# Kernel tuning notes

Hardware: AMD Instinct MI355X
Metric: run time of the kernel (lower is better)

The kernel has to match this reference:

```python
import jax, jax.numpy as jnp
import numpy as np
import math

SR = 16000
WIN = 320
HOP = 160
NFFT = 512
NMEL = 64
PREEMPH = 0.97
LOG_GUARD = 2.0 ** (-24)
PAD_TO = 16
EPS = 1e-5  # CONSTANT added to std


def _slaney_mel_fbanks(sr=SR, n_fft=NFFT, n_mels=NMEL, fmin=0.0, fmax=8000.0):
    """Replicates torchaudio.functional.melscale_fbanks(norm='slaney', mel_scale='slaney').
    Returns [n_mels, n_freqs] (already transposed like the torch buffer `fb`)."""
    n_freqs = n_fft // 2 + 1
    all_freqs = np.linspace(0.0, sr / 2.0, n_freqs)
    f_sp = 200.0 / 3.0
    min_log_hz = 1000.0
    min_log_mel = min_log_hz / f_sp
    logstep = math.log(6.4) / 27.0

    def hz2mel(f):
        f = np.asarray(f, dtype=np.float64)
        return np.where(f >= min_log_hz,
                        min_log_mel + np.log(np.maximum(f, 1e-10) / min_log_hz) / logstep,
                        f / f_sp)

    def mel2hz(m):
        m = np.asarray(m, dtype=np.float64)
        return np.where(m >= min_log_mel,
                        min_log_hz * np.exp(logstep * (m - min_log_mel)),
                        f_sp * m)

    m_pts = np.linspace(hz2mel(fmin), hz2mel(fmax), n_mels + 2)
    f_pts = mel2hz(m_pts)                       # [n_mels+2]
    f_diff = f_pts[1:] - f_pts[:-1]             # [n_mels+1]
    slopes = f_pts[None, :] - all_freqs[:, None]  # [n_freqs, n_mels+2]
    down = -slopes[:, :-2] / f_diff[:-1]
    up = slopes[:, 2:] / f_diff[1:]
    fb = np.maximum(0.0, np.minimum(down, up))  # [n_freqs, n_mels]
    enorm = 2.0 / (f_pts[2:] - f_pts[:-2])      # slaney area normalization
    fb = fb * enorm[None, :]
    return fb.T.astype(np.float32)              # [n_mels, n_freqs]


def _hann_window_padded(win_length=WIN, n_fft=NFFT):
    # the window symmetrically to n_fft.
    w = np.hanning(win_length).astype(np.float32)
    left = (n_fft - win_length) // 2
    out = np.zeros(n_fft, dtype=np.float32)
    out[left:left + win_length] = w
    return out


def setup_inputs() -> dict:
    key = jax.random.key(0)
    kx, kl = jax.random.split(key)
    B, L = 32, 256000
    x = jax.random.normal(kx, (B, L), dtype=jnp.float32)
    # ragged valid lengths in [L/2, L] (plenty of frames per feature)
    seq_len = jax.random.randint(kl, (B,), L // 2, L + 1, dtype=jnp.int32)
    window = jnp.asarray(_hann_window_padded())       # [NFFT]
    fb = jnp.asarray(_slaney_mel_fbanks())            # [NMEL, NFFT//2+1]
    return {"x": x, "seq_len": seq_len, "window": window, "fb": fb}


def _forward(x, seq_len, window, fb):
    B, L = x.shape
    # get_seq_len: pad_amount = 2*(n_fft//2); floor((L + pad - n_fft)/hop) + 1
    feat_len = (seq_len + NFFT - NFFT) // HOP + 1     # = seq_len // HOP + 1
    # pre-emphasis
    x = jnp.concatenate([x[:, :1], x[:, 1:] - PREEMPH * x[:, :-1]], axis=1)
    # STFT, center=True reflect padding (eval mode: no dither)
    pad = NFFT // 2
    xp = jnp.pad(x, ((0, 0), (pad, pad)), mode='reflect')
    T = L // HOP + 1                                  # 1601 frames
    idx = jnp.arange(T)[:, None] * HOP + jnp.arange(NFFT)[None, :]
    frames = xp[:, idx] * window                      # [B, T, NFFT]
    spec = jnp.fft.rfft(frames, axis=-1)              # [B, T, F]
    # magnitude then mag_power=2 -> power spectrum (guard=0 since use_grads=False)
    pow_spec = spec.real ** 2 + spec.imag ** 2        # [B, T, F]
    mel = jnp.einsum('mf,btf->bmt', fb, pow_spec)     # [B, NMEL, T]
    logmel = jnp.log(mel + LOG_GUARD)
    # per_feature masked normalization (torch.std is unbiased -> /(n-1)), std += 1e-5
    mask = (jnp.arange(T)[None, :] < feat_len[:, None])          # [B, T]
    m = mask[:, None, :].astype(logmel.dtype)                    # [B, 1, T]
    n = feat_len.astype(logmel.dtype)[:, None, None]
    mean = jnp.sum(logmel * m, axis=2, keepdims=True) / n
    var = jnp.sum(((logmel - mean) * m) ** 2, axis=2, keepdims=True) / (n - 1.0)
    std = jnp.sqrt(var) + EPS
    out = (logmel - mean) / std
    # fill padding frames with pad_value=0
    out = jnp.where(m > 0, out, 0.0)
    # pad time dim to a multiple of pad_to=16 with pad_value
    pad_amt = (-T) % PAD_TO
    out = jnp.pad(out, ((0, 0), (0, 0), (0, pad_amt)), constant_values=0.0)
    return out, feat_len


def reference(x, seq_len, window, fb):
    return _forward(x, seq_len, window, fb)
```

## Files before the change

kernel.cpp:

```cpp
#include <hip/hip_runtime.h>
#include <math.h>

#define L_IN 256000
#define T_FR 1601
#define T_PAD 1616
#define NMEL_K 64
#define F_BINS 257
#define HOP_K 160
#define PRE_E 0.97f
#define LOG_GUARD_K 5.9604644775390625e-08f
#define FPB 16
#define CONC 4
#define GROUPS 101
#define SPAN 2912

__device__ __forceinline__ float2 cmulf(float2 a, float2 b) {
  return make_float2(a.x * b.x - a.y * b.y, a.x * b.y + a.y * b.x);
}

__device__ __forceinline__ float dpp_xor1(float x) {
  return __int_as_float(__builtin_amdgcn_mov_dpp(__float_as_int(x), 0xB1, 0xF, 0xF, true));
}
__device__ __forceinline__ float dpp_xor2(float x) {
  return __int_as_float(__builtin_amdgcn_mov_dpp(__float_as_int(x), 0x4E, 0xF, 0xF, true));
}

__global__ void prep_kernel(const float* __restrict__ fb, float* __restrict__ fbc,
                            int* __restrict__ loAl, float* __restrict__ rsum,
                            float* __restrict__ rsumsq) {
  const int m = blockIdx.x;
  const int t = threadIdx.x;
  if (t < 32) {
    rsum[m * 32 + t] = 0.0f;
    rsumsq[m * 32 + t] = 0.0f;
  }
  int first = 512, last = -1;
  for (int c = 0; c < 5; ++c) {
    int f = t + 64 * c;
    if (f < F_BINS) {
      float v = fb[m * F_BINS + f];
      if (v > 0.0f) { first = min(first, f); last = max(last, f); }
    }
  }
  for (int off = 32; off > 0; off >>= 1) {
    first = min(first, __shfl_xor(first, off));
    last = max(last, __shfl_xor(last, off));
  }
  int lo = (first <= last) ? first : 0;
  int lastv = (first <= last) ? last : 0;
  int la = lo & ~3;
  if (t == 0) loAl[m] = la;
  if (t < 32) {
    int f = la + t;
    float v = (f >= lo && f <= lastv && f < F_BINS) ? fb[m * F_BINS + f] : 0.0f;
    fbc[m * 32 + t] = v;
  }
}

#define FFT_STAGE(I, PR, PI)                                        \
  {                                                                 \
    const int H__ = 32 >> (I);                                      \
    const bool hi__ = (lane & H__) != 0;                            \
    const float cc__ = stc[I], ss__ = sts[I];                       \
    _Pragma("unroll")                                               \
    for (int r = 0; r < 4; ++r) {                                   \
      float tr = (PR), ti = (PI);                                   \
      float sr = Br[r] + tr, si = Bi[r] + ti;                       \
      float dr = tr - Br[r], di = ti - Bi[r];                       \
      float pr = dr * cc__ - di * ss__, pi = dr * ss__ + di * cc__; \
      Br[r] = hi__ ? pr : sr;                                       \
      Bi[r] = hi__ ? pi : si;                                       \
    }                                                               \
  }

__global__ void __launch_bounds__(256) frame_fft_mel_kernel(
    const float* __restrict__ x, const int* __restrict__ seq_len,
    const float* __restrict__ window, const float* __restrict__ fbc,
    const int* __restrict__ loAl, float* __restrict__ out,
    float* __restrict__ rsum, float* __restrict__ rsumsq) {
  __shared__ __align__(16) float xs[SPAN];
  __shared__ __align__(16) float pw[CONC][288];
  __shared__ float outm[NMEL_K][FPB + 1];

  const int tid = threadIdx.x;
  const int w = tid >> 6;
  const int lane = tid & 63;
  const int b = blockIdx.x / GROUPS;
  const int g = blockIdx.x - b * GROUPS;
  const int t0 = g * FPB;
  const float* xb = x + (size_t)b * L_IN;
  const int base = t0 * HOP_K - 256;
  const int fl = seq_len[b] / HOP_K + 1;

  if (base >= 0 && base + SPAN <= L_IN) {
    const float4* xb4 = (const float4*)(xb + base);
    float4* xs4 = (float4*)xs;
    for (int s4 = tid; s4 < SPAN / 4; s4 += 256) {
      float4 cur = xb4[s4];
      float prev = xb[base + 4 * s4 - 1];
      float4 o;
      o.x = fmaf(-PRE_E, prev, cur.x);
      o.y = fmaf(-PRE_E, cur.x, cur.y);
      o.z = fmaf(-PRE_E, cur.y, cur.z);
      o.w = fmaf(-PRE_E, cur.z, cur.w);
      xs4[s4] = o;
    }
  } else {
    for (int n = tid; n < SPAN; n += 256) {
      int i = base + n;
      i = (i < 0) ? -i : i;
      i = (i >= L_IN) ? (2 * L_IN - 2 - i) : i;
      xs[n] = (i == 0) ? xb[0] : fmaf(-PRE_E, xb[i - 1], xb[i]);
    }
  }

  if (lane >= 33 && lane < 64) pw[w][224 + lane] = 0.0f;

  const int sig = __builtin_bitreverse32(lane) >> 26;
  float wr[4], wi[4];
#pragma unroll
  for (int q = 0; q < 4; ++q) {
    float2 wv = *(const float2*)(window + 2 * (lane + 64 * q));
    wr[q] = wv.x; wi[q] = wv.y;
  }
  float2 tw1, tw2, tw3;
  {
    float a = -0.024543692606170259f * (float)lane;
    __sincosf(a, &tw1.y, &tw1.x);
    tw2 = cmulf(tw1, tw1);
    tw3 = cmulf(tw2, tw1);
  }
  float stc[6], sts[6];
#pragma unroll
  for (int i = 0; i < 6; ++i) {
    int H = 32 >> i;
    int p = lane & (H - 1);
    float a = -3.14159265358979323846f * (float)p / (float)H;
    __sincosf(a, &sts[i], &stc[i]);
  }
  float cu[4], su[4];
  {
    float a = -0.049087385212340519f * (float)sig;
    float cb, sb;
    __sincosf(a, &sb, &cb);
    const float C[4] = {1.0f, 0.99992470183914454f, 0.99969881869620425f, 0.99932238458834954f};
    const float S[4] = {0.0f, 0.01227153828571993f, 0.02454122852291229f, 0.03680722294135883f};
#pragma unroll
    for (int r = 0; r < 4; ++r) {
      cu[r] = cb * C[r] + sb * S[r];
      su[r] = sb * C[r] - cb * S[r];
    }
  }
  const int idx0 = __builtin_bitreverse32((64 - sig) & 63) >> 26;
  const int la = loAl[lane];
  const float4* fr4 = (const float4*)fbc + lane * 8;

  __syncthreads();

  float sm = 0.0f, ssq = 0.0f;

  for (int c = 0; c < FPB / CONC; ++c) {
    const int j = c * CONC + w;
    const int off = j * HOP_K;

    float Br[4], Bi[4];
    {
      float zr[4], zi[4];
#pragma unroll
      for (int q = 0; q < 4; ++q) {
        float2 v = *(const float2*)(xs + off + 2 * (lane + 64 * q));
        zr[q] = v.x * wr[q];
        zi[q] = v.y * wi[q];
      }
      float e0r = zr[0] + zr[2], e0i = zi[0] + zi[2];
      float e1r = zr[1] + zr[3], e1i = zi[1] + zi[3];
      float d0r = zr[0] - zr[2], d0i = zi[0] - zi[2];
      float d1r = zr[1] - zr[3], d1i = zi[1] - zi[3];
      Br[0] = e0r + e1r; Bi[0] = e0i + e1i;
      float A2r = e0r - e1r, A2i = e0i - e1i;
      float A1r = d0r + d1i, A1i = d0i - d1r;
      float A3r = d0r - d1i, A3i = d0i + d1r;
      Br[1] = A1r * tw1.x - A1i * tw1.y; Bi[1] = A1r * tw1.y + A1i * tw1.x;
      Br[2] = A2r * tw2.x - A2i * tw2.y; Bi[2] = A2r * tw2.y + A2i * tw2.x;
      Br[3] = A3r * tw3.x - A3i * tw3.y; Bi[3] = A3r * tw3.y + A3i * tw3.x;
    }

    FFT_STAGE(0, __shfl_xor(Br[r], 32), __shfl_xor(Bi[r], 32));
    FFT_STAGE(1, __shfl_xor(Br[r], 16), __shfl_xor(Bi[r], 16));
    FFT_STAGE(2, __shfl_xor(Br[r], 8), __shfl_xor(Bi[r], 8));
    FFT_STAGE(3, __shfl_xor(Br[r], 4), __shfl_xor(Bi[r], 4));
    FFT_STAGE(4, dpp_xor2(Br[r]), dpp_xor2(Bi[r]));
    FFT_STAGE(5, dpp_xor1(Br[r]), dpp_xor1(Bi[r]));

    {
      float q3r = __shfl_xor(Br[3], 63), q3i = __shfl_xor(Bi[3], 63);
      float q2r = __shfl_xor(Br[2], 63), q2i = __shfl_xor(Bi[2], 63);
      float q1r = __shfl_xor(Br[1], 63), q1i = __shfl_xor(Bi[1], 63);
      float q0r = __shfl(Br[0], idx0), q0i = __shfl(Bi[0], idx0);
      float qr[4] = {q0r, q3r, q2r, q1r};
      float qi_[4] = {q0i, q3i, q2i, q1i};
      float pv[4];
#pragma unroll
      for (int r = 0; r < 4; ++r) {
        float Er = 0.5f * (Br[r] + qr[r]);
        float Ei = 0.5f * (Bi[r] - qi_[r]);
        float Or = 0.5f * (Bi[r] + qi_[r]);
        float Oi = 0.5f * (qr[r] - Br[r]);
        float Xr = Er + cu[r] * Or - su[r] * Oi;
        float Xi = Ei + cu[r] * Oi + su[r] * Or;
        pv[r] = Xr * Xr + Xi * Xi;
      }
      ((float4*)pw[w])[sig] = make_float4(pv[0], pv[1], pv[2], pv[3]);
      if (lane == 0) { float d = Br[0] - Bi[0]; pw[w][256] = d * d; }
    }
    __builtin_amdgcn_wave_barrier();

    {
      const float4* pq = (const float4*)pw[w] + (la >> 2);
      float acc = 0.0f;
#pragma unroll
      for (int jj = 0; jj < 8; ++jj) {
        float4 wq = fr4[jj];
        float4 p = pq[jj];
        acc = fmaf(wq.x, p.x, acc);
        acc = fmaf(wq.y, p.y, acc);
        acc = fmaf(wq.z, p.z, acc);
        acc = fmaf(wq.w, p.w, acc);
      }
      float lv = __logf(acc + LOG_GUARD_K);
      outm[lane][j] = lv;
      if (t0 + j < fl) { sm += lv; ssq = fmaf(lv, lv, ssq); }
    }
    __builtin_amdgcn_wave_barrier();
  }

  pw[w][lane] = sm;
  pw[w][64 + lane] = ssq;

  __syncthreads();

#pragma unroll
  for (int p = 0; p < 4; ++p) {
    int row = p * 16 + (tid >> 4);
    int jj = tid & 15;
    int t = t0 + jj;
    if (t < T_FR)
      out[((size_t)(b << 6) + row) * T_PAD + t] = outm[row][jj];
  }

  if (tid < 64) {
    float s0 = pw[0][tid] + pw[1][tid] + pw[2][tid] + pw[3][tid];
    float q0 = pw[0][64 + tid] + pw[1][64 + tid] + pw[2][64 + tid] + pw[3][64 + tid];
    atomicAdd(&rsum[(b << 6) + tid], s0);
    atomicAdd(&rsumsq[(b << 6) + tid], q0);
  }
}

__global__ void __launch_bounds__(256) norm_elem_kernel(
    const int* __restrict__ seq_len, const float* __restrict__ rsum,
    const float* __restrict__ rsumsq, float* __restrict__ out,
    float* __restrict__ fl_out) {
  const int cidx = blockIdx.x * 256 + threadIdx.x;
  const int bm = cidx / (T_PAD / 4);
  const int c4 = cidx - bm * (T_PAD / 4);
  const int b = bm >> 6;
  const int fl = seq_len[b] / HOP_K + 1;
  const float n = (float)fl;
  float s = rsum[bm], ssq = rsumsq[bm];
  float mean = s / n;
  float var = (ssq - s * mean) / (n - 1.0f);
  float istd = 1.0f / (sqrtf(var) + 1e-5f);
  float4* rowp = (float4*)(out + (size_t)bm * T_PAD);
  float4 v = rowp[c4];
  int t = 4 * c4;
  float4 o;
  o.x = (t < fl) ? (v.x - mean) * istd : 0.0f;
  o.y = (t + 1 < fl) ? (v.y - mean) * istd : 0.0f;
  o.z = (t + 2 < fl) ? (v.z - mean) * istd : 0.0f;
  o.w = (t + 3 < fl) ? (v.w - mean) * istd : 0.0f;
  rowp[c4] = o;
  if (blockIdx.x == 0 && threadIdx.x < 32)
    fl_out[threadIdx.x] = (float)(seq_len[threadIdx.x] / HOP_K + 1);
}

extern "C" void kernel_launch(void* const* d_in, const int* in_sizes, int n_in,
                              void* d_out, int out_size, void* d_ws, size_t ws_size,
                              hipStream_t stream) {
  const float* x = (const float*)d_in[0];
  const int* seq_len = (const int*)d_in[1];
  const float* window = (const float*)d_in[2];
  const float* fb = (const float*)d_in[3];
  float* out = (float*)d_out;
  float* fl_out = out + (size_t)32 * NMEL_K * T_PAD;
  float* fbc = (float*)d_ws;
  int* loAl = (int*)((char*)d_ws + 8192);
  float* rsum = (float*)((char*)d_ws + 8448);
  float* rsumsq = (float*)((char*)d_ws + 16640);

  prep_kernel<<<NMEL_K, 64, 0, stream>>>(fb, fbc, loAl, rsum, rsumsq);
  frame_fft_mel_kernel<<<32 * GROUPS, 256, 0, stream>>>(x, seq_len, window, fbc,
                                                        loAl, out, rsum, rsumsq);
  norm_elem_kernel<<<(32 * NMEL_K * T_PAD / 4) / 256, 256, 0, stream>>>(
      seq_len, rsum, rsumsq, out, fl_out);
}
```

Baseline: 126.6 us.

## Process two frames per wave concurrently and swizzle power-spectrum LDS layout

Each wave now computes two frames' FFTs together, interleaving their butterfly stages to hide cross-lane shuffle latency, with the loop count halved. The power-spectrum scratch buffer is doubled and its float4 slots are XOR-swizzled to reduce LDS bank conflicts on the mel dot products. Launch bounds now request 4 blocks per CU. This raises register pressure, which could limit occupancy or cause spills.

```diff
diff --git a/kernel.cpp b/kernel.cpp
--- a/kernel.cpp
+++ b/kernel.cpp
@@ -25,6 +25,8 @@
   return __int_as_float(__builtin_amdgcn_mov_dpp(__float_as_int(x), 0x4E, 0xF, 0xF, true));
 }
 
+#define PW_SWZ(q) ((q) ^ (((q) >> 3) & 7))
+
 __global__ void prep_kernel(const float* __restrict__ fb, float* __restrict__ fbc,
                             int* __restrict__ loAl, float* __restrict__ rsum,
                             float* __restrict__ rsumsq) {
@@ -57,29 +59,32 @@
   }
 }
 
-#define FFT_STAGE(I, PR, PI)                                        \
-  {                                                                 \
-    const int H__ = 32 >> (I);                                      \
-    const bool hi__ = (lane & H__) != 0;                            \
-    const float cc__ = stc[I], ss__ = sts[I];                       \
-    _Pragma("unroll")                                               \
-    for (int r = 0; r < 4; ++r) {                                   \
-      float tr = (PR), ti = (PI);                                   \
-      float sr = Br[r] + tr, si = Bi[r] + ti;                       \
-      float dr = tr - Br[r], di = ti - Bi[r];                       \
-      float pr = dr * cc__ - di * ss__, pi = dr * ss__ + di * cc__; \
-      Br[r] = hi__ ? pr : sr;                                       \
-      Bi[r] = hi__ ? pi : si;                                       \
-    }                                                               \
-  }
-
-__global__ void __launch_bounds__(256) frame_fft_mel_kernel(
+#define FFT_STAGE(I, PR, PI)                                          \
+  {                                                                   \
+    const int H__ = 32 >> (I);                                        \
+    const bool hi__ = (lane & H__) != 0;                              \
+    const float cc__ = stc[I], ss__ = sts[I];                         \
+    _Pragma("unroll")                                                 \
+    for (int f = 0; f < 2; ++f) {                                     \
+      _Pragma("unroll")                                               \
+      for (int r = 0; r < 4; ++r) {                                   \
+        float tr = (PR), ti = (PI);                                   \
+        float sr = Br[f][r] + tr, si = Bi[f][r] + ti;                 \
+        float dr = tr - Br[f][r], di = ti - Bi[f][r];                 \
+        float pr = dr * cc__ - di * ss__, pi = dr * ss__ + di * cc__; \
+        Br[f][r] = hi__ ? pr : sr;                                    \
+        Bi[f][r] = hi__ ? pi : si;                                    \
+      }                                                               \
+    }                                                                 \
+  }
+
+__global__ void __launch_bounds__(256, 4) frame_fft_mel_kernel(
     const float* __restrict__ x, const int* __restrict__ seq_len,
     const float* __restrict__ window, const float* __restrict__ fbc,
     const int* __restrict__ loAl, float* __restrict__ out,
     float* __restrict__ rsum, float* __restrict__ rsumsq) {
   __shared__ __align__(16) float xs[SPAN];
-  __shared__ __align__(16) float pw[CONC][288];
+  __shared__ __align__(16) float pw[2 * CONC][288];
   __shared__ float outm[NMEL_K][FPB + 1];
 
   const int tid = threadIdx.x;
@@ -114,7 +119,10 @@
     }
   }
 
-  if (lane >= 33 && lane < 64) pw[w][224 + lane] = 0.0f;
+  if (lane >= 33) {
+    pw[2 * w][224 + lane] = 0.0f;
+    pw[2 * w + 1][224 + lane] = 0.0f;
+  }
 
   const int sig = __builtin_bitreverse32(lane) >> 26;
   float wr[4], wi[4];
@@ -154,17 +162,19 @@
   const int idx0 = __builtin_bitreverse32((64 - sig) & 63) >> 26;
   const int la = loAl[lane];
   const float4* fr4 = (const float4*)fbc + lane * 8;
+  const int sigswz = PW_SWZ(sig);
 
   __syncthreads();
 
   float sm = 0.0f, ssq = 0.0f;
 
-  for (int c = 0; c < FPB / CONC; ++c) {
-    const int j = c * CONC + w;
-    const int off = j * HOP_K;
-
-    float Br[4], Bi[4];
-    {
+  for (int c = 0; c < 2; ++c) {
+    const int jA = c * 8 + 2 * w;
+
+    float Br[2][4], Bi[2][4];
+#pragma unroll
+    for (int f = 0; f < 2; ++f) {
+      const int off = (jA + f) * HOP_K;
       float zr[4], zi[4];
 #pragma unroll
       for (int q = 0; q < 4; ++q) {
@@ -176,66 +186,78 @@
       float e1r = zr[1] + zr[3], e1i = zi[1] + zi[3];
       float d0r = zr[0] - zr[2], d0i = zi[0] - zi[2];
       float d1r = zr[1] - zr[3], d1i = zi[1] - zi[3];
-      Br[0] = e0r + e1r; Bi[0] = e0i + e1i;
+      Br[f][0] = e0r + e1r; Bi[f][0] = e0i + e1i;
       float A2r = e0r - e1r, A2i = e0i - e1i;
       float A1r = d0r + d1i, A1i = d0i - d1r;
       float A3r = d0r - d1i, A3i = d0i + d1r;
-      Br[1] = A1r * tw1.x - A1i * tw1.y; Bi[1] = A1r * tw1.y + A1i * tw1.x;
-      Br[2] = A2r * tw2.x - A2i * tw2.y; Bi[2] = A2r * tw2.y + A2i * tw2.x;
-      Br[3] = A3r * tw3.x - A3i * tw3.y; Bi[3] = A3r * tw3.y + A3i * tw3.x;
-    }
-
-    FFT_STAGE(0, __shfl_xor(Br[r], 32), __shfl_xor(Bi[r], 32));
-    FFT_STAGE(1, __shfl_xor(Br[r], 16), __shfl_xor(Bi[r], 16));
-    FFT_STAGE(2, __shfl_xor(Br[r], 8), __shfl_xor(Bi[r], 8));
-    FFT_STAGE(3, __shfl_xor(Br[r], 4), __shfl_xor(Bi[r], 4));
-    FFT_STAGE(4, dpp_xor2(Br[r]), dpp_xor2(Bi[r]));
-    FFT_STAGE(5, dpp_xor1(Br[r]), dpp_xor1(Bi[r]));
-
-    {
-      float q3r = __shfl_xor(Br[3], 63), q3i = __shfl_xor(Bi[3], 63);
-      float q2r = __shfl_xor(Br[2], 63), q2i = __shfl_xor(Bi[2], 63);
-      float q1r = __shfl_xor(Br[1], 63), q1i = __shfl_xor(Bi[1], 63);
-      float q0r = __shfl(Br[0], idx0), q0i = __shfl(Bi[0], idx0);
+      Br[f][1] = A1r * tw1.x - A1i * tw1.y; Bi[f][1] = A1r * tw1.y + A1i * tw1.x;
+      Br[f][2] = A2r * tw2.x - A2i * tw2.y; Bi[f][2] = A2r * tw2.y + A2i * tw2.x;
+      Br[f][3] = A3r * tw3.x - A3i * tw3.y; Bi[f][3] = A3r * tw3.y + A3i * tw3.x;
+    }
+
+    FFT_STAGE(0, __shfl_xor(Br[f][r], 32), __shfl_xor(Bi[f][r], 32));
+    FFT_STAGE(1, __shfl_xor(Br[f][r], 16), __shfl_xor(Bi[f][r], 16));
+    FFT_STAGE(2, __shfl_xor(Br[f][r], 8), __shfl_xor(Bi[f][r], 8));
+    FFT_STAGE(3, __shfl_xor(Br[f][r], 4), __shfl_xor(Bi[f][r], 4));
+    FFT_STAGE(4, dpp_xor2(Br[f][r]), dpp_xor2(Bi[f][r]));
+    FFT_STAGE(5, dpp_xor1(Br[f][r]), dpp_xor1(Bi[f][r]));
+
+#pragma unroll
+    for (int f = 0; f < 2; ++f) {
+      float q3r = __shfl_xor(Br[f][3], 63), q3i = __shfl_xor(Bi[f][3], 63);
+      float q2r = __shfl_xor(Br[f][2], 63), q2i = __shfl_xor(Bi[f][2], 63);
+      float q1r = __shfl_xor(Br[f][1], 63), q1i = __shfl_xor(Bi[f][1], 63);
+      float q0r = __shfl(Br[f][0], idx0), q0i = __shfl(Bi[f][0], idx0);
       float qr[4] = {q0r, q3r, q2r, q1r};
       float qi_[4] = {q0i, q3i, q2i, q1i};
       float pv[4];
 #pragma unroll
       for (int r = 0; r < 4; ++r) {
-        float Er = 0.5f * (Br[r] + qr[r]);
-        float Ei = 0.5f * (Bi[r] - qi_[r]);
-        float Or = 0.5f * (Bi[r] + qi_[r]);
-        float Oi = 0.5f * (qr[r] - Br[r]);
+        float Er = 0.5f * (Br[f][r] + qr[r]);
+        float Ei = 0.5f * (Bi[f][r] - qi_[r]);
+        float Or = 0.5f * (Bi[f][r] + qi_[r]);
+        float Oi = 0.5f * (qr[r] - Br[f][r]);
         float Xr = Er + cu[r] * Or - su[r] * Oi;
         float Xi = Ei + cu[r] * Oi + su[r] * Or;
         pv[r] = Xr * Xr + Xi * Xi;
       }
-      ((float4*)pw[w])[sig] = make_float4(pv[0], pv[1], pv[2], pv[3]);
-      if (lane == 0) { float d = Br[0] - Bi[0]; pw[w][256] = d * d; }
+      ((float4*)pw[2 * w + f])[sigswz] = make_float4(pv[0], pv[1], pv[2], pv[3]);
+      if (lane == 0) { float d = Br[f][0] - Bi[f][0]; pw[2 * w + f][256] = d * d; }
     }
     __builtin_amdgcn_wave_barrier();
 
     {
-      const float4* pq = (const float4*)pw[w] + (la >> 2);
-      float acc = 0.0f;
+      const float4* pqA = (const float4*)pw[2 * w];
+      const float4* pqB = (const float4*)pw[2 * w + 1];
+      const int la4 = la >> 2;
+      float accA = 0.0f, accB = 0.0f;
 #pragma unroll
       for (int jj = 0; jj < 8; ++jj) {
         float4 wq = fr4[jj];
-        float4 p = pq[jj];
-        acc = fmaf(wq.x, p.x, acc);
-        acc = fmaf(wq.y, p.y, acc);
-        acc = fmaf(wq.z, p.z, acc);
-        acc = fmaf(wq.w, p.w, acc);
+        int q = PW_SWZ(la4 + jj);
+        float4 pA = pqA[q];
+        float4 pB = pqB[q];
+        accA = fmaf(wq.x, pA.x, accA);
+        accA = fmaf(wq.y, pA.y, accA);
+        accA = fmaf(wq.z, pA.z, accA);
+        accA = fmaf(wq.w, pA.w, accA);
+        accB = fmaf(wq.x, pB.x, accB);
+        accB = fmaf(wq.y, pB.y, accB);
+        accB = fmaf(wq.z, pB.z, accB);
+        accB = fmaf(wq.w, pB.w, accB);
       }
-      float lv = __logf(acc + LOG_GUARD_K);
-      outm[lane][j] = lv;
-      if (t0 + j < fl) { sm += lv; ssq = fmaf(lv, lv, ssq); }
+      float lvA = __logf(accA + LOG_GUARD_K);
+      float lvB = __logf(accB + LOG_GUARD_K);
+      outm[lane][jA] = lvA;
+      outm[lane][jA + 1] = lvB;
+      if (t0 + jA < fl) { sm += lvA; ssq = fmaf(lvA, lvA, ssq); }
+      if (t0 + jA + 1 < fl) { sm += lvB; ssq = fmaf(lvB, lvB, ssq); }
     }
     __builtin_amdgcn_wave_barrier();
   }
 
-  pw[w][lane] = sm;
-  pw[w][64 + lane] = ssq;
+  pw[2 * w][lane] = sm;
+  pw[2 * w][64 + lane] = ssq;
 
   __syncthreads();
 
@@ -249,8 +271,8 @@
   }
 
   if (tid < 64) {
-    float s0 = pw[0][tid] + pw[1][tid] + pw[2][tid] + pw[3][tid];
-    float q0 = pw[0][64 + tid] + pw[1][64 + tid] + pw[2][64 + tid] + pw[3][64 + tid];
+    float s0 = pw[0][tid] + pw[2][tid] + pw[4][tid] + pw[6][tid];
+    float q0 = pw[0][64 + tid] + pw[2][64 + tid] + pw[4][64 + tid] + pw[6][64 + tid];
     atomicAdd(&rsum[(b << 6) + tid], s0);
     atomicAdd(&rsumsq[(b << 6) + tid], q0);
   }
```

New measurement: 172.1 us. 1.36x slower.
